# Kernel tuning notes

Measured on AMD Instinct MI355X. Metric: run time of the kernel, lower is better.

## Reference

```python
import jax, jax.numpy as jnp
import numpy as np

B, T_IN, F, U = 4096, 256, 32, 64
OUT_STEPS = 24


def _lstm_step(x, h, c, W, R, b):
    # Keras LSTMCell: gates z = x@W + h@R + b, split as [i, f, g, o]
    z = x @ W + h @ R + b  # [B, 4U]
    i, f, g, o = jnp.split(z, 4, axis=-1)
    i = jax.nn.sigmoid(i)
    f = jax.nn.sigmoid(f)
    g = jnp.tanh(g)
    o = jax.nn.sigmoid(o)
    c_new = f * c + i * g
    h_new = o * jnp.tanh(c_new)
    return h_new, c_new


def setup_inputs() -> dict:
    key = jax.random.key(0)
    ks = jax.random.split(key, 9)
    s_in = 1.0 / np.sqrt(F)
    s_hid = 1.0 / np.sqrt(U)
    return {
        "inputs": jax.random.normal(ks[0], (B, T_IN, F), jnp.float32),
        "W1": jax.random.normal(ks[1], (F, 4 * U), jnp.float32) * s_in,
        "U1": jax.random.normal(ks[2], (U, 4 * U), jnp.float32) * s_hid,
        "b1": jnp.zeros((4 * U,), jnp.float32),
        "W2": jax.random.normal(ks[3], (F, 4 * U), jnp.float32) * s_in,
        "U2": jax.random.normal(ks[4], (U, 4 * U), jnp.float32) * s_hid,
        "b2": jnp.zeros((4 * U,), jnp.float32),
        "Wd": jax.random.normal(ks[5], (U, F), jnp.float32) * s_hid,
        "bd": jnp.zeros((F,), jnp.float32),
    }


def reference(inputs, W1, U1, b1, W2, U2, b2, Wd, bd):
    batch = inputs.shape[0]
    units = U1.shape[0]
    h0 = jnp.zeros((batch, units), inputs.dtype)
    c0 = jnp.zeros((batch, units), inputs.dtype)

    # ---- warmup: run lstm_cell_warmup over the input sequence ----
    def warm_step(carry, x_t):
        h, c = carry
        h, c = _lstm_step(x_t, h, c, W1, U1, b1)
        return (h, c), None

    (h, c), _ = jax.lax.scan(warm_step, (h0, c0), jnp.swapaxes(inputs, 0, 1))
    pred0 = h @ Wd + bd  # [B, F]

    def dec_step(carry, _):
        pred, h, c = carry
        h, c = _lstm_step(pred, h, c, W2, U2, b2)
        pred = h @ Wd + bd
        return (pred, h, c), pred

    _, preds_rest = jax.lax.scan(dec_step, (pred0, h, c), None, length=OUT_STEPS - 1)
    preds = jnp.concatenate([pred0[None], preds_rest], axis=0)  # [T_out, B, F]
    return jnp.transpose(preds, (1, 0, 2))  # [B, T_out, F]
```

## Files before the change

### kernel.cpp

```cpp
#include <hip/hip_runtime.h>
#include <math.h>

#define T_STEPS 256
#define Fdim 32
#define Udim 64
#define G4 256
#define OUT_STEPS 24
#define ROWS 16
#define NBLK 256
#define NTHR 512
#define HBS 72
#define CHUNK 32
#define NCHUNK 8
#define LOG2E 1.4426950408889634f

typedef __attribute__((ext_vector_type(8))) short short8;
typedef __attribute__((ext_vector_type(4))) float f32x4;

__device__ __forceinline__ short f2bf(float f) {
    union { float f; unsigned u; } v; v.f = f;
    unsigned r = v.u + 0x7FFFu + ((v.u >> 16) & 1u);
    return (short)(r >> 16);
}
__device__ __forceinline__ float bf2f(short s) {
    union { unsigned u; float f; } v; v.u = ((unsigned)(unsigned short)s) << 16;
    return v.f;
}
__device__ __forceinline__ float frcp(float v) { return __builtin_amdgcn_rcpf(v); }
__device__ __forceinline__ float fexp2(float v) { return __builtin_amdgcn_exp2f(v); }

__device__ __forceinline__ unsigned pkbf(float lo, float hi) {
    unsigned r;
    asm("v_cvt_pk_bf16_f32 %0, %1, %2" : "=v"(r) : "v"(lo), "v"(hi));
    return r;
}

__device__ __forceinline__ float cell_h(const f32x4 a, float& cst) {
    float A  = fexp2(-a[0]);
    float Bv = fexp2(a[2]);
    float rf = frcp(1.0f + fexp2(-a[1]));
    float ig = (Bv - 1.0f) * frcp((1.0f + A) * (1.0f + Bv));
    cst = fmaf(cst, rf, ig);
    float C  = fexp2(-a[3]);
    float D  = fexp2(2.0f * LOG2E * cst);
    return (D - 1.0f) * frcp((1.0f + C) * (1.0f + D));
}

#define BAR() asm volatile("s_waitcnt lgkmcnt(0)\n\ts_barrier" ::: "memory")

__global__ __launch_bounds__(NTHR, 1)
void lstm_v6(const float* __restrict__ x,
             const float* __restrict__ W1, const float* __restrict__ U1, const float* __restrict__ b1,
             const float* __restrict__ W2, const float* __restrict__ U2, const float* __restrict__ b2,
             const float* __restrict__ Wd, const float* __restrict__ bd,
             float* __restrict__ out)
{
    __shared__ __align__(16) short hb[2][ROWS][HBS];
    __shared__ __align__(16) short xs[CHUNK][ROWS][HBS];
    __shared__ float WdL[Udim * Fdim];

    const int tid = threadIdx.x;
    const int l   = tid & 63;
    const int w   = tid >> 6;
    const int q   = l >> 4;
    const int m   = l & 15;
    const int brow = blockIdx.x * ROWS;

    const int f4 = tid & 7;
    const int tt = (tid >> 3) & 31;
    const int r0 = tid >> 8;
    float4 pf[8];
#pragma unroll
    for (int i = 0; i < 8; ++i)
        pf[i] = *(const float4*)&x[((size_t)(brow + r0 + 2 * i) * T_STEPS + tt) * Fdim + f4 * 4];

    short8 wa1[2][3], wa2[2][3];
    f32x4 bs1[2], bs2[2];
#pragma unroll
    for (int nt = 0; nt < 2; ++nt) {
        const int unit_a = w * 8 + (m >> 2) * 2 + nt;
        const int gate_a = m & 3;
        const int col = gate_a * 64 + unit_a;
        const float sA = (gate_a == 2) ? 2.0f * LOG2E : LOG2E;
#pragma unroll
        for (int kt = 0; kt < 3; ++kt) {
            short8 fa, fb;
#pragma unroll
            for (int j = 0; j < 8; ++j) {
                const int k = kt * 32 + q * 8 + j;
                float v1 = (k < Udim) ? U1[k * G4 + col] : W1[(k - Udim) * G4 + col];
                float v2 = (k < Udim) ? U2[k * G4 + col] : W2[(k - Udim) * G4 + col];
                fa[j] = f2bf(v1 * sA);
                fb[j] = f2bf(v2 * sA);
            }
            wa1[nt][kt] = fa;
            wa2[nt][kt] = fb;
        }
        const int unit_d = w * 8 + q * 2 + nt;
#pragma unroll
        for (int g = 0; g < 4; ++g) {
            const float sD = (g == 2) ? 2.0f * LOG2E : LOG2E;
            bs1[nt][g] = b1[g * 64 + unit_d] * sD;
            bs2[nt][g] = b2[g * 64 + unit_d] * sD;
        }
    }

    const int sr = tid >> 5;
    const int sc = tid & 31;
    const float bdv = bd[sc];
    const int hw = w * 8 + q * 2;

    for (int idx = tid; idx < 2 * ROWS * HBS; idx += NTHR) ((short*)hb)[idx] = 0;
    for (int idx = tid; idx < Udim * Fdim; idx += NTHR) WdL[idx] = Wd[idx];
    float cst[2] = {0.f, 0.f};

    for (int c = 0; c < NCHUNK; ++c) {
#pragma unroll
        for (int i = 0; i < 8; ++i) {
            uint2 pk;
            pk.x = pkbf(pf[i].x, pf[i].y);
            pk.y = pkbf(pf[i].z, pf[i].w);
            *(uint2*)&xs[tt][r0 + 2 * i][f4 * 4] = pk;
        }
        if (c + 1 < NCHUNK) {
#pragma unroll
            for (int i = 0; i < 8; ++i)
                pf[i] = *(const float4*)&x[((size_t)(brow + r0 + 2 * i) * T_STEPS + ((c + 1) * CHUNK + tt)) * Fdim + f4 * 4];
        }
        BAR();

#pragma unroll 2
        for (int t2 = 0; t2 < CHUNK; ++t2) {
            const int p = t2 & 1;

            const short8 b0  = *(const short8*)&hb[p][m][q * 8];
            const short8 b1v = *(const short8*)&hb[p][m][32 + q * 8];
            const short8 b2v = *(const short8*)&xs[t2][m][q * 8];

            f32x4 a0 = __builtin_amdgcn_mfma_f32_16x16x32_bf16(wa1[0][0], b0, bs1[0], 0, 0, 0);
            f32x4 a1 = __builtin_amdgcn_mfma_f32_16x16x32_bf16(wa1[1][0], b0, bs1[1], 0, 0, 0);
            a0 = __builtin_amdgcn_mfma_f32_16x16x32_bf16(wa1[0][1], b1v, a0, 0, 0, 0);
            a1 = __builtin_amdgcn_mfma_f32_16x16x32_bf16(wa1[1][1], b1v, a1, 0, 0, 0);
            a0 = __builtin_amdgcn_mfma_f32_16x16x32_bf16(wa1[0][2], b2v, a0, 0, 0, 0);
            a1 = __builtin_amdgcn_mfma_f32_16x16x32_bf16(wa1[1][2], b2v, a1, 0, 0, 0);

            const float h0 = cell_h(a0, cst[0]);
            const float h1 = cell_h(a1, cst[1]);
            *(unsigned*)&hb[1 - p][m][hw] = pkbf(h0, h1);
            BAR();
        }
    }

    {
        float acc = bdv;
#pragma unroll
        for (int kb = 0; kb < 8; ++kb) {
            short8 h8 = *(const short8*)&hb[0][sr][kb * 8];
#pragma unroll
            for (int j = 0; j < 8; ++j)
                acc = fmaf(bf2f(h8[j]), WdL[(kb * 8 + j) * Fdim + sc], acc);
        }
        out[(size_t)(brow + sr) * (OUT_STEPS * Fdim) + sc] = acc;
        xs[0][sr][sc] = f2bf(acc);
    }
    BAR();

    int dp = 0;
    for (int s = 1; s < OUT_STEPS; ++s) {
        const short8 b0  = *(const short8*)&hb[dp][m][q * 8];
        const short8 b1v = *(const short8*)&hb[dp][m][32 + q * 8];
        const short8 b2v = *(const short8*)&xs[0][m][q * 8];

        f32x4 a0 = __builtin_amdgcn_mfma_f32_16x16x32_bf16(wa2[0][0], b0, bs2[0], 0, 0, 0);
        f32x4 a1 = __builtin_amdgcn_mfma_f32_16x16x32_bf16(wa2[1][0], b0, bs2[1], 0, 0, 0);
        a0 = __builtin_amdgcn_mfma_f32_16x16x32_bf16(wa2[0][1], b1v, a0, 0, 0, 0);
        a1 = __builtin_amdgcn_mfma_f32_16x16x32_bf16(wa2[1][1], b1v, a1, 0, 0, 0);
        a0 = __builtin_amdgcn_mfma_f32_16x16x32_bf16(wa2[0][2], b2v, a0, 0, 0, 0);
        a1 = __builtin_amdgcn_mfma_f32_16x16x32_bf16(wa2[1][2], b2v, a1, 0, 0, 0);

        const float h0 = cell_h(a0, cst[0]);
        const float h1 = cell_h(a1, cst[1]);
        *(unsigned*)&hb[1 - dp][m][hw] = pkbf(h0, h1);
        BAR();

        float dacc = bdv;
#pragma unroll
        for (int kb = 0; kb < 8; ++kb) {
            short8 h8 = *(const short8*)&hb[1 - dp][sr][kb * 8];
#pragma unroll
            for (int j = 0; j < 8; ++j)
                dacc = fmaf(bf2f(h8[j]), WdL[(kb * 8 + j) * Fdim + sc], dacc);
        }
        out[(size_t)(brow + sr) * (OUT_STEPS * Fdim) + s * Fdim + sc] = dacc;
        xs[0][sr][sc] = f2bf(dacc);
        BAR();
        dp = 1 - dp;
    }
}

extern "C" void kernel_launch(void* const* d_in, const int* in_sizes, int n_in,
                              void* d_out, int out_size, void* d_ws, size_t ws_size,
                              hipStream_t stream) {
    (void)in_sizes; (void)n_in; (void)out_size; (void)d_ws; (void)ws_size;
    const float* x  = (const float*)d_in[0];
    const float* W1 = (const float*)d_in[1];
    const float* U1 = (const float*)d_in[2];
    const float* b1 = (const float*)d_in[3];
    const float* W2 = (const float*)d_in[4];
    const float* U2 = (const float*)d_in[5];
    const float* b2 = (const float*)d_in[6];
    const float* Wd = (const float*)d_in[7];
    const float* bd = (const float*)d_in[8];
    float* out = (float*)d_out;

    lstm_v6<<<dim3(NBLK), dim3(NTHR), 0, stream>>>(
        x, W1, U1, b1, W2, U2, b2, Wd, bd, out);
}
```

Before: 306.8 us.

## Swizzle LDS layout and prefetch next-step x operand ahead of barrier

Applies an XOR swizzle on the column index (by row bit 3) to the h and x LDS buffers to reduce bank conflicts in the row-padded layout. In the warmup loop, the x operand for the next timestep is loaded before the barrier, and the MFMA chain starts with the x term so it does not depend on the freshly written h. In the decode loop, the h operands are loaded before the barrier of the previous step. The goal is to shorten the serial per-step latency of the recurrence, at the cost of extra registers and added index arithmetic.

After: 309.4 us. No clear change (+0.8%).

```diff
diff --git a/kernel.cpp b/kernel.cpp
--- a/kernel.cpp
+++ b/kernel.cpp
@@ -35,6 +35,8 @@
     return r;
 }
 
+__device__ __forceinline__ int swz(int col, int row) { return col ^ ((row & 8) << 2); }
+
 __device__ __forceinline__ float cell_h(const f32x4 a, float& cst) {
     float A  = fexp2(-a[0]);
     float Bv = fexp2(a[2]);
@@ -48,8 +50,10 @@
 
 #define BAR() asm volatile("s_waitcnt lgkmcnt(0)\n\ts_barrier" ::: "memory")
 
+#define MFMA __builtin_amdgcn_mfma_f32_16x16x32_bf16
+
 __global__ __launch_bounds__(NTHR, 1)
-void lstm_v6(const float* __restrict__ x,
+void lstm_v7(const float* __restrict__ x,
              const float* __restrict__ W1, const float* __restrict__ U1, const float* __restrict__ b1,
              const float* __restrict__ W2, const float* __restrict__ U2, const float* __restrict__ b2,
              const float* __restrict__ Wd, const float* __restrict__ bd,
@@ -109,6 +113,7 @@
     const int sc = tid & 31;
     const float bdv = bd[sc];
     const int hw = w * 8 + q * 2;
+    const int bswz = (m & 8) << 2;
 
     for (int idx = tid; idx < 2 * ROWS * HBS; idx += NTHR) ((short*)hb)[idx] = 0;
     for (int idx = tid; idx < Udim * Fdim; idx += NTHR) WdL[idx] = Wd[idx];
@@ -117,10 +122,11 @@
     for (int c = 0; c < NCHUNK; ++c) {
 #pragma unroll
         for (int i = 0; i < 8; ++i) {
+            const int row = r0 + 2 * i;
             uint2 pk;
             pk.x = pkbf(pf[i].x, pf[i].y);
             pk.y = pkbf(pf[i].z, pf[i].w);
-            *(uint2*)&xs[tt][r0 + 2 * i][f4 * 4] = pk;
+            *(uint2*)&xs[tt][row][swz(f4 * 4, row)] = pk;
         }
         if (c + 1 < NCHUNK) {
 #pragma unroll
@@ -128,71 +134,78 @@
                 pf[i] = *(const float4*)&x[((size_t)(brow + r0 + 2 * i) * T_STEPS + ((c + 1) * CHUNK + tt)) * Fdim + f4 * 4];
         }
         BAR();
+
+        short8 b2p = *(const short8*)&xs[0][m][(q * 8) ^ bswz];
 
 #pragma unroll 2
         for (int t2 = 0; t2 < CHUNK; ++t2) {
             const int p = t2 & 1;
 
-            const short8 b0  = *(const short8*)&hb[p][m][q * 8];
-            const short8 b1v = *(const short8*)&hb[p][m][32 + q * 8];
-            const short8 b2v = *(const short8*)&xs[t2][m][q * 8];
-
-            f32x4 a0 = __builtin_amdgcn_mfma_f32_16x16x32_bf16(wa1[0][0], b0, bs1[0], 0, 0, 0);
-            f32x4 a1 = __builtin_amdgcn_mfma_f32_16x16x32_bf16(wa1[1][0], b0, bs1[1], 0, 0, 0);
-            a0 = __builtin_amdgcn_mfma_f32_16x16x32_bf16(wa1[0][1], b1v, a0, 0, 0, 0);
-            a1 = __builtin_amdgcn_mfma_f32_16x16x32_bf16(wa1[1][1], b1v, a1, 0, 0, 0);
-            a0 = __builtin_amdgcn_mfma_f32_16x16x32_bf16(wa1[0][2], b2v, a0, 0, 0, 0);
-            a1 = __builtin_amdgcn_mfma_f32_16x16x32_bf16(wa1[1][2], b2v, a1, 0, 0, 0);
+            const short8 b2v = b2p;
+            const short8 b0  = *(const short8*)&hb[p][m][(q * 8) ^ bswz];
+            const short8 b1v = *(const short8*)&hb[p][m][(32 + q * 8) ^ bswz];
+
+            f32x4 a0 = MFMA(wa1[0][2], b2v, bs1[0], 0, 0, 0);
+            f32x4 a1 = MFMA(wa1[1][2], b2v, bs1[1], 0, 0, 0);
+            a0 = MFMA(wa1[0][0], b0, a0, 0, 0, 0);
+            a1 = MFMA(wa1[1][0], b0, a1, 0, 0, 0);
+            a0 = MFMA(wa1[0][1], b1v, a0, 0, 0, 0);
+            a1 = MFMA(wa1[1][1], b1v, a1, 0, 0, 0);
 
             const float h0 = cell_h(a0, cst[0]);
             const float h1 = cell_h(a1, cst[1]);
-            *(unsigned*)&hb[1 - p][m][hw] = pkbf(h0, h1);
+            *(unsigned*)&hb[1 - p][m][hw ^ bswz] = pkbf(h0, h1);
+            if (t2 + 1 < CHUNK)
+                b2p = *(const short8*)&xs[t2 + 1][m][(q * 8) ^ bswz];
             BAR();
         }
     }
 
+    short8 b0p, b1p;
     {
         float acc = bdv;
 #pragma unroll
         for (int kb = 0; kb < 8; ++kb) {
-            short8 h8 = *(const short8*)&hb[0][sr][kb * 8];
+            short8 h8 = *(const short8*)&hb[0][sr][swz(kb * 8, sr)];
 #pragma unroll
             for (int j = 0; j < 8; ++j)
                 acc = fmaf(bf2f(h8[j]), WdL[(kb * 8 + j) * Fdim + sc], acc);
         }
         out[(size_t)(brow + sr) * (OUT_STEPS * Fdim) + sc] = acc;
-        xs[0][sr][sc] = f2bf(acc);
+        xs[0][sr][swz(sc, sr)] = f2bf(acc);
+        b0p = *(const short8*)&hb[0][m][(q * 8) ^ bswz];
+        b1p = *(const short8*)&hb[0][m][(32 + q * 8) ^ bswz];
     }
     BAR();
 
     int dp = 0;
     for (int s = 1; s < OUT_STEPS; ++s) {
-        const short8 b0  = *(const short8*)&hb[dp][m][q * 8];
-        const short8 b1v = *(const short8*)&hb[dp][m][32 + q * 8];
-        const short8 b2v = *(const short8*)&xs[0][m][q * 8];
-
-        f32x4 a0 = __builtin_amdgcn_mfma_f32_16x16x32_bf16(wa2[0][0], b0, bs2[0], 0, 0, 0);
-        f32x4 a1 = __builtin_amdgcn_mfma_f32_16x16x32_bf16(wa2[1][0], b0, bs2[1], 0, 0, 0);
-        a0 = __builtin_amdgcn_mfma_f32_16x16x32_bf16(wa2[0][1], b1v, a0, 0, 0, 0);
-        a1 = __builtin_amdgcn_mfma_f32_16x16x32_bf16(wa2[1][1], b1v, a1, 0, 0, 0);
-        a0 = __builtin_amdgcn_mfma_f32_16x16x32_bf16(wa2[0][2], b2v, a0, 0, 0, 0);
-        a1 = __builtin_amdgcn_mfma_f32_16x16x32_bf16(wa2[1][2], b2v, a1, 0, 0, 0);
+        const short8 b2v = *(const short8*)&xs[0][m][(q * 8) ^ bswz];
+
+        f32x4 a0 = MFMA(wa2[0][0], b0p, bs2[0], 0, 0, 0);
+        f32x4 a1 = MFMA(wa2[1][0], b0p, bs2[1], 0, 0, 0);
+        a0 = MFMA(wa2[0][1], b1p, a0, 0, 0, 0);
+        a1 = MFMA(wa2[1][1], b1p, a1, 0, 0, 0);
+        a0 = MFMA(wa2[0][2], b2v, a0, 0, 0, 0);
+        a1 = MFMA(wa2[1][2], b2v, a1, 0, 0, 0);
 
         const float h0 = cell_h(a0, cst[0]);
         const float h1 = cell_h(a1, cst[1]);
-        *(unsigned*)&hb[1 - dp][m][hw] = pkbf(h0, h1);
+        *(unsigned*)&hb[1 - dp][m][hw ^ bswz] = pkbf(h0, h1);
         BAR();
 
         float dacc = bdv;
 #pragma unroll
         for (int kb = 0; kb < 8; ++kb) {
-            short8 h8 = *(const short8*)&hb[1 - dp][sr][kb * 8];
+            short8 h8 = *(const short8*)&hb[1 - dp][sr][swz(kb * 8, sr)];
 #pragma unroll
             for (int j = 0; j < 8; ++j)
                 dacc = fmaf(bf2f(h8[j]), WdL[(kb * 8 + j) * Fdim + sc], dacc);
         }
         out[(size_t)(brow + sr) * (OUT_STEPS * Fdim) + s * Fdim + sc] = dacc;
-        xs[0][sr][sc] = f2bf(dacc);
+        xs[0][sr][swz(sc, sr)] = f2bf(dacc);
+        b0p = *(const short8*)&hb[1 - dp][m][(q * 8) ^ bswz];
+        b1p = *(const short8*)&hb[1 - dp][m][(32 + q * 8) ^ bswz];
         BAR();
         dp = 1 - dp;
     }
@@ -213,6 +226,6 @@
     const float* bd = (const float*)d_in[8];
     float* out = (float*)d_out;
 
-    lstm_v6<<<dim3(NBLK), dim3(NTHR), 0, stream>>>(
+    lstm_v7<<<dim3(NBLK), dim3(NTHR), 0, stream>>>(
         x, W1, U1, b1, W2, U2, b2, Wd, bd, out);
 }
```

## Double threads per block so each wave computes one unit tile of gates

Applied to the files above, without the earlier changes.

Raises the block from 8 to 16 waves so each wave issues one MFMA chain instead of two, halving per-wave serial work on the recurrent critical path. It also prefetches the next timestep's input fragment from shared memory ahead of the barrier, and preloads decode-phase hidden fragments before the barrier. In exchange, barriers now span 16 waves and each wave does a scalar 2-byte store for h. Only the first 512 threads run the dense projection.

Result: no change. 304.1 us (-0.9%).

```diff
diff --git a/kernel.cpp b/kernel.cpp
--- a/kernel.cpp
+++ b/kernel.cpp
@@ -8,7 +8,7 @@
 #define OUT_STEPS 24
 #define ROWS 16
 #define NBLK 256
-#define NTHR 512
+#define NTHR 1024
 #define HBS 72
 #define CHUNK 32
 #define NCHUNK 8
@@ -48,8 +48,10 @@
 
 #define BAR() asm volatile("s_waitcnt lgkmcnt(0)\n\ts_barrier" ::: "memory")
 
+#define MFMA __builtin_amdgcn_mfma_f32_16x16x32_bf16
+
 __global__ __launch_bounds__(NTHR, 1)
-void lstm_v6(const float* __restrict__ x,
+void lstm_v8(const float* __restrict__ x,
              const float* __restrict__ W1, const float* __restrict__ U1, const float* __restrict__ b1,
              const float* __restrict__ W2, const float* __restrict__ U2, const float* __restrict__ b2,
              const float* __restrict__ Wd, const float* __restrict__ bd,
@@ -69,16 +71,15 @@
     const int f4 = tid & 7;
     const int tt = (tid >> 3) & 31;
     const int r0 = tid >> 8;
-    float4 pf[8];
-#pragma unroll
-    for (int i = 0; i < 8; ++i)
-        pf[i] = *(const float4*)&x[((size_t)(brow + r0 + 2 * i) * T_STEPS + tt) * Fdim + f4 * 4];
-
-    short8 wa1[2][3], wa2[2][3];
-    f32x4 bs1[2], bs2[2];
-#pragma unroll
-    for (int nt = 0; nt < 2; ++nt) {
-        const int unit_a = w * 8 + (m >> 2) * 2 + nt;
+    float4 pf[4];
+#pragma unroll
+    for (int i = 0; i < 4; ++i)
+        pf[i] = *(const float4*)&x[((size_t)(brow + r0 + 4 * i) * T_STEPS + tt) * Fdim + f4 * 4];
+
+    short8 wa1[3], wa2[3];
+    f32x4 bs1, bs2;
+    {
+        const int unit_a = (w >> 1) * 8 + (m >> 2) * 2 + (w & 1);
         const int gate_a = m & 3;
         const int col = gate_a * 64 + unit_a;
         const float sA = (gate_a == 2) ? 2.0f * LOG2E : LOG2E;
@@ -93,65 +94,66 @@
                 fa[j] = f2bf(v1 * sA);
                 fb[j] = f2bf(v2 * sA);
             }
-            wa1[nt][kt] = fa;
-            wa2[nt][kt] = fb;
-        }
-        const int unit_d = w * 8 + q * 2 + nt;
-#pragma unroll
-        for (int g = 0; g < 4; ++g) {
-            const float sD = (g == 2) ? 2.0f * LOG2E : LOG2E;
-            bs1[nt][g] = b1[g * 64 + unit_d] * sD;
-            bs2[nt][g] = b2[g * 64 + unit_d] * sD;
-        }
+            wa1[kt] = fa;
+            wa2[kt] = fb;
+        }
+    }
+    const int unit_d = (w >> 1) * 8 + q * 2 + (w & 1);
+#pragma unroll
+    for (int g = 0; g < 4; ++g) {
+        const float sD = (g == 2) ? 2.0f * LOG2E : LOG2E;
+        bs1[g] = b1[g * 64 + unit_d] * sD;
+        bs2[g] = b2[g * 64 + unit_d] * sD;
     }
 
     const int sr = tid >> 5;
     const int sc = tid & 31;
     const float bdv = bd[sc];
-    const int hw = w * 8 + q * 2;
 
     for (int idx = tid; idx < 2 * ROWS * HBS; idx += NTHR) ((short*)hb)[idx] = 0;
     for (int idx = tid; idx < Udim * Fdim; idx += NTHR) WdL[idx] = Wd[idx];
-    float cst[2] = {0.f, 0.f};
+    float cst = 0.f;
 
     for (int c = 0; c < NCHUNK; ++c) {
 #pragma unroll
-        for (int i = 0; i < 8; ++i) {
+        for (int i = 0; i < 4; ++i) {
+            const int row = r0 + 4 * i;
             uint2 pk;
             pk.x = pkbf(pf[i].x, pf[i].y);
             pk.y = pkbf(pf[i].z, pf[i].w);
-            *(uint2*)&xs[tt][r0 + 2 * i][f4 * 4] = pk;
+            *(uint2*)&xs[tt][row][f4 * 4] = pk;
         }
         if (c + 1 < NCHUNK) {
 #pragma unroll
-            for (int i = 0; i < 8; ++i)
-                pf[i] = *(const float4*)&x[((size_t)(brow + r0 + 2 * i) * T_STEPS + ((c + 1) * CHUNK + tt)) * Fdim + f4 * 4];
+            for (int i = 0; i < 4; ++i)
+                pf[i] = *(const float4*)&x[((size_t)(brow + r0 + 4 * i) * T_STEPS + ((c + 1) * CHUNK + tt)) * Fdim + f4 * 4];
         }
         BAR();
+
+        short8 b2p = *(const short8*)&xs[0][m][q * 8];
 
 #pragma unroll 2
         for (int t2 = 0; t2 < CHUNK; ++t2) {
             const int p = t2 & 1;
 
+            const short8 b2v = b2p;
             const short8 b0  = *(const short8*)&hb[p][m][q * 8];
             const short8 b1v = *(const short8*)&hb[p][m][32 + q * 8];
-            const short8 b2v = *(const short8*)&xs[t2][m][q * 8];
-
-            f32x4 a0 = __builtin_amdgcn_mfma_f32_16x16x32_bf16(wa1[0][0], b0, bs1[0], 0, 0, 0);
-            f32x4 a1 = __builtin_amdgcn_mfma_f32_16x16x32_bf16(wa1[1][0], b0, bs1[1], 0, 0, 0);
-            a0 = __builtin_amdgcn_mfma_f32_16x16x32_bf16(wa1[0][1], b1v, a0, 0, 0, 0);
-            a1 = __builtin_amdgcn_mfma_f32_16x16x32_bf16(wa1[1][1], b1v, a1, 0, 0, 0);
-            a0 = __builtin_amdgcn_mfma_f32_16x16x32_bf16(wa1[0][2], b2v, a0, 0, 0, 0);
-            a1 = __builtin_amdgcn_mfma_f32_16x16x32_bf16(wa1[1][2], b2v, a1, 0, 0, 0);
-
-            const float h0 = cell_h(a0, cst[0]);
-            const float h1 = cell_h(a1, cst[1]);
-            *(unsigned*)&hb[1 - p][m][hw] = pkbf(h0, h1);
+
+            f32x4 a = MFMA(wa1[2], b2v, bs1, 0, 0, 0);
+            a = MFMA(wa1[0], b0, a, 0, 0, 0);
+            a = MFMA(wa1[1], b1v, a, 0, 0, 0);
+
+            const float h0 = cell_h(a, cst);
+            hb[1 - p][m][unit_d] = f2bf(h0);
+            if (t2 + 1 < CHUNK)
+                b2p = *(const short8*)&xs[t2 + 1][m][q * 8];
             BAR();
         }
     }
 
-    {
+    short8 b0p, b1p;
+    if (tid < 512) {
         float acc = bdv;
 #pragma unroll
         for (int kb = 0; kb < 8; ++kb) {
@@ -163,36 +165,36 @@
         out[(size_t)(brow + sr) * (OUT_STEPS * Fdim) + sc] = acc;
         xs[0][sr][sc] = f2bf(acc);
     }
+    b0p = *(const short8*)&hb[0][m][q * 8];
+    b1p = *(const short8*)&hb[0][m][32 + q * 8];
     BAR();
 
     int dp = 0;
     for (int s = 1; s < OUT_STEPS; ++s) {
-        const short8 b0  = *(const short8*)&hb[dp][m][q * 8];
-        const short8 b1v = *(const short8*)&hb[dp][m][32 + q * 8];
         const short8 b2v = *(const short8*)&xs[0][m][q * 8];
 
-        f32x4 a0 = __builtin_amdgcn_mfma_f32_16x16x32_bf16(wa2[0][0], b0, bs2[0], 0, 0, 0);
-        f32x4 a1 = __builtin_amdgcn_mfma_f32_16x16x32_bf16(wa2[1][0], b0, bs2[1], 0, 0, 0);
-        a0 = __builtin_amdgcn_mfma_f32_16x16x32_bf16(wa2[0][1], b1v, a0, 0, 0, 0);
-        a1 = __builtin_amdgcn_mfma_f32_16x16x32_bf16(wa2[1][1], b1v, a1, 0, 0, 0);
-        a0 = __builtin_amdgcn_mfma_f32_16x16x32_bf16(wa2[0][2], b2v, a0, 0, 0, 0);
-        a1 = __builtin_amdgcn_mfma_f32_16x16x32_bf16(wa2[1][2], b2v, a1, 0, 0, 0);
-
-        const float h0 = cell_h(a0, cst[0]);
-        const float h1 = cell_h(a1, cst[1]);
-        *(unsigned*)&hb[1 - dp][m][hw] = pkbf(h0, h1);
+        f32x4 a = MFMA(wa2[0], b0p, bs2, 0, 0, 0);
+        a = MFMA(wa2[1], b1p, a, 0, 0, 0);
+        a = MFMA(wa2[2], b2v, a, 0, 0, 0);
+
+        const float h0 = cell_h(a, cst);
+        hb[1 - dp][m][unit_d] = f2bf(h0);
         BAR();
 
-        float dacc = bdv;
-#pragma unroll
-        for (int kb = 0; kb < 8; ++kb) {
-            short8 h8 = *(const short8*)&hb[1 - dp][sr][kb * 8];
-#pragma unroll
-            for (int j = 0; j < 8; ++j)
-                dacc = fmaf(bf2f(h8[j]), WdL[(kb * 8 + j) * Fdim + sc], dacc);
-        }
-        out[(size_t)(brow + sr) * (OUT_STEPS * Fdim) + s * Fdim + sc] = dacc;
-        xs[0][sr][sc] = f2bf(dacc);
+        if (tid < 512) {
+            float dacc = bdv;
+#pragma unroll
+            for (int kb = 0; kb < 8; ++kb) {
+                short8 h8 = *(const short8*)&hb[1 - dp][sr][kb * 8];
+#pragma unroll
+                for (int j = 0; j < 8; ++j)
+                    dacc = fmaf(bf2f(h8[j]), WdL[(kb * 8 + j) * Fdim + sc], dacc);
+            }
+            out[(size_t)(brow + sr) * (OUT_STEPS * Fdim) + s * Fdim + sc] = dacc;
+            xs[0][sr][sc] = f2bf(dacc);
+        }
+        b0p = *(const short8*)&hb[1 - dp][m][q * 8];
+        b1p = *(const short8*)&hb[1 - dp][m][32 + q * 8];
         BAR();
         dp = 1 - dp;
     }
@@ -213,6 +215,6 @@
     const float* bd = (const float*)d_in[8];
     float* out = (float*)d_out;
 
-    lstm_v6<<<dim3(NBLK), dim3(NTHR), 0, stream>>>(
+    lstm_v8<<<dim3(NBLK), dim3(NTHR), 0, stream>>>(
         x, W1, U1, b1, W2, U2, b2, Wd, bd, out);
 }
```
